# Optimization experiments

Measured on AMD Instinct MI355X. Metric: run time of the kernel, lower is better.

Reference implementation:

```python
import jax, jax.numpy as jnp
import numpy as np

N = 50000      # nodes
E = 800000     # edges (avg degree 16)
D = 96         # input_size == output_size
C = 10         # n_class
STEPS = 4      # num_layers -> GGNN propagation steps


def setup_inputs() -> dict:
    key = jax.random.key(0)
    ks = jax.random.split(key, 12)
    s = 1.0 / np.sqrt(D)
    return {
        "x": jax.random.normal(ks[0], (N, D), dtype=jnp.float32),
        "src": jax.random.randint(ks[1], (E,), 0, N, dtype=jnp.int32),
        "dst": jax.random.randint(ks[2], (E,), 0, N, dtype=jnp.int32),
        # edge message transform (DGL GatedGraphConv: Linear(out, out) per etype, 1 etype)
        "W_e": jax.random.normal(ks[3], (D, D), dtype=jnp.float32) * s,
        "b_e": jax.random.normal(ks[4], (D,), dtype=jnp.float32) * s,
        # GRUCell params (torch layout: rows ordered r, z, n)
        "W_ih": jax.random.normal(ks[5], (3 * D, D), dtype=jnp.float32) * s,
        "W_hh": jax.random.normal(ks[6], (3 * D, D), dtype=jnp.float32) * s,
        "b_ih": jax.random.normal(ks[7], (3 * D,), dtype=jnp.float32) * s,
        "b_hh": jax.random.normal(ks[8], (3 * D,), dtype=jnp.float32) * s,
        # classifier head
        "W_fc": jax.random.normal(ks[9], (C, D), dtype=jnp.float32) * s,
        "b_fc": jax.random.normal(ks[10], (C,), dtype=jnp.float32) * s,
    }


def _gru_cell(a, h, W_ih, W_hh, b_ih, b_hh):
    # torch.nn.GRUCell math; gate order r, z, n
    gx = a @ W_ih.T + b_ih            # [N, 3D]
    gh = h @ W_hh.T + b_hh            # [N, 3D]
    xr, xz, xn = jnp.split(gx, 3, axis=-1)
    hr, hz, hn = jnp.split(gh, 3, axis=-1)
    r = jax.nn.sigmoid(xr + hr)
    z = jax.nn.sigmoid(xz + hz)
    n = jnp.tanh(xn + r * hn)
    return (1.0 - z) * n + z * h


def reference(x, src, dst, W_e, b_e, W_ih, W_hh, b_ih, b_hh, W_fc, b_fc):
    h = x  # in_feats == out_feats, no padding needed
    for _ in range(STEPS):
        m = h @ W_e.T + b_e                                  # per-node transform [N, D]
        a = jax.ops.segment_sum(m[src], dst, num_segments=N) # gather + scatter-add [N, D]
        h = _gru_cell(a, h, W_ih, W_hh, b_ih, b_hh)
    logits = jax.nn.elu(h) @ W_fc.T + b_fc                   # [N, C]
    return logits
```

## Files before the change

kernel.cpp:

```cpp
#include <hip/hip_runtime.h>

static constexpr int D = 96;
static constexpr int G3 = 3 * D;
static constexpr int NSTEPS = 4;
static constexpr int NT = 18;
static constexpr int SCAN_BLK = 1024;
static constexpr int SLP = 104;
static constexpr int PLS = 97;
static constexpr int PLANE = 16 * PLS;

typedef __attribute__((ext_vector_type(8))) _Float16 f16x8;
typedef __attribute__((ext_vector_type(4))) _Float16 f16x4;
typedef __attribute__((ext_vector_type(4))) float f32x4;

__device__ __forceinline__ f16x8 load_a_frag(const _Float16* __restrict__ base,
                                             int r0, int lane, int kc) {
  int row = r0 + (lane & 15);
  int k0 = kc * 32 + ((lane >> 4) << 3);
  return *(const f16x8*)(base + (size_t)row * D + k0);
}

__device__ __forceinline__ f16x8 load_b_swz(const _Float16* __restrict__ W,
                                            int t, int kc, int lane) {
  return *(const f16x8*)(W + (((size_t)t * 3 + kc) * 64 + lane) * 8);
}


__global__ void convert_x_kernel(const float* __restrict__ x,
                                 _Float16* __restrict__ h, int total4) {
  int i = blockIdx.x * blockDim.x + threadIdx.x;
  if (i >= total4) return;
  float4 v = ((const float4*)x)[i];
  f16x4 o;
  o[0] = (_Float16)v.x; o[1] = (_Float16)v.y;
  o[2] = (_Float16)v.z; o[3] = (_Float16)v.w;
  *(f16x4*)(h + (size_t)i * 4) = o;
}

__global__ void compute_wx_kernel(const float* __restrict__ Wih,
                                  const float* __restrict__ We,
                                  const float* __restrict__ be,
                                  float* __restrict__ Wx,
                                  float* __restrict__ bxe) {
  int idx = blockIdx.x * blockDim.x + threadIdx.x;
  if (idx < G3 * D) {
    int r = idx / D, k = idx - r * D;
    float acc = 0.f;
    for (int c = 0; c < D; ++c) acc += Wih[r * D + c] * We[c * D + k];
    Wx[idx] = acc;
  } else if (idx < G3 * D + G3) {
    int r = idx - G3 * D;
    float acc = 0.f;
    for (int c = 0; c < D; ++c) acc += Wih[r * D + c] * be[c];
    bxe[r] = acc;
  }
}

__global__ void swizzle_f16_kernel(const float* __restrict__ Wx,
                                   const float* __restrict__ Whh,
                                   _Float16* __restrict__ WxF,
                                   _Float16* __restrict__ WhhF) {
  int idx = blockIdx.x * blockDim.x + threadIdx.x;
  if (idx >= 2 * NT * 3 * 64) return;
  int mat = idx / (NT * 3 * 64);
  int rem = idx - mat * (NT * 3 * 64);
  int t = rem / (3 * 64);
  int rem2 = rem - t * (3 * 64);
  int kc = rem2 >> 6;
  int lane = rem2 & 63;
  int c = t * 16 + (lane & 15);
  int k0 = kc * 32 + ((lane >> 4) << 3);
  const float* W = mat ? Whh : Wx;
  _Float16* dF = mat ? WhhF : WxF;
  f16x8 o;
#pragma unroll
  for (int j = 0; j < 8; ++j) o[j] = (_Float16)W[(size_t)c * D + k0 + j];
  *(f16x8*)(dF + (((size_t)t * 3 + kc) * 64 + lane) * 8) = o;
}


__global__ void hist_kernel(const int* __restrict__ dst, int* __restrict__ counts, int E) {
  int e = blockIdx.x * blockDim.x + threadIdx.x;
  if (e < E) atomicAdd(&counts[dst[e]], 1);
}

__global__ void partial_sum_kernel(const int* __restrict__ counts,
                                   int* __restrict__ blk_sums, int n) {
  __shared__ int red[256];
  int base = blockIdx.x * SCAN_BLK;
  int tid = threadIdx.x;
  int s = 0;
#pragma unroll
  for (int j = 0; j < 4; ++j) {
    int i = base + j * 256 + tid;
    if (i < n) s += counts[i];
  }
  red[tid] = s;
  __syncthreads();
  for (int off = 128; off > 0; off >>= 1) {
    if (tid < off) red[tid] += red[tid + off];
    __syncthreads();
  }
  if (tid == 0) blk_sums[blockIdx.x] = red[0];
}

__global__ void scan_offsets_kernel(const int* __restrict__ blk_sums,
                                    int* __restrict__ blk_off,
                                    int* __restrict__ row_ptr, int nb, int n) {
  __shared__ int lds[64];
  int tid = threadIdx.x;
  if (tid < nb) lds[tid] = blk_sums[tid];
  __syncthreads();
  if (tid == 0) {
    int run = 0;
    for (int i = 0; i < nb; ++i) { blk_off[i] = run; run += lds[i]; }
    row_ptr[n] = run;
  }
}

__global__ void block_scan_kernel(const int* __restrict__ counts,
                                  const int* __restrict__ blk_off,
                                  int* __restrict__ row_ptr, int n) {
  __shared__ int red[256];
  int base = blockIdx.x * SCAN_BLK;
  int tid = threadIdx.x;
  int i0 = base + tid * 4;
  int v0 = 0, v1 = 0, v2 = 0, v3 = 0;
  if (i0 + 3 < n) {
    int4 c = *(const int4*)(counts + i0);
    v0 = c.x; v1 = c.y; v2 = c.z; v3 = c.w;
  } else {
    if (i0 < n) v0 = counts[i0];
    if (i0 + 1 < n) v1 = counts[i0 + 1];
    if (i0 + 2 < n) v2 = counts[i0 + 2];
  }
  int tsum = v0 + v1 + v2 + v3;
  red[tid] = tsum;
  __syncthreads();
  for (int off = 1; off < 256; off <<= 1) {
    int t = (tid >= off) ? red[tid - off] : 0;
    __syncthreads();
    red[tid] += t;
    __syncthreads();
  }
  int excl = blk_off[blockIdx.x] + red[tid] - tsum;
  if (i0 < n) row_ptr[i0] = excl;
  if (i0 + 1 < n) row_ptr[i0 + 1] = excl + v0;
  if (i0 + 2 < n) row_ptr[i0 + 2] = excl + v0 + v1;
  if (i0 + 3 < n) row_ptr[i0 + 3] = excl + v0 + v1 + v2;
}

__global__ void fill_kernel(const int* __restrict__ src, const int* __restrict__ dst,
                            const int* __restrict__ row_ptr,
                            int* __restrict__ fillc,
                            unsigned short* __restrict__ csr_src, int E) {
  int e = blockIdx.x * blockDim.x + threadIdx.x;
  if (e >= E) return;
  int t = dst[e];
  int pos = row_ptr[t] + atomicAdd(&fillc[t], 1);
  csr_src[pos] = (unsigned short)src[e];
}


__device__ __forceinline__ void gru_epilogue(const float* lds,
                                             const _Float16* __restrict__ h,
                                             _Float16* __restrict__ hout,
                                             const int* __restrict__ row_ptr,
                                             const float* __restrict__ bxe,
                                             const float* __restrict__ bih,
                                             const float* __restrict__ bhh,
                                             int base_row, int tid) {
#pragma unroll
  for (int j = 0; j < 4; ++j) {
    int e = tid + j * 384;
    int row = e / D;
    int col = e - row * D;
    int grow = base_row + row;
    int a = row * PLS + col;
    float degf = (float)(row_ptr[grow + 1] - row_ptr[grow]);
    float R  = lds[a] + lds[PLANE + a];
    float Z  = lds[2 * PLANE + a] + lds[3 * PLANE + a];
    float XN = lds[4 * PLANE + a];
    float HN = lds[5 * PLANE + a];
    float rg = 1.0f / (1.0f + __expf(-(R + bih[col] + bhh[col] + degf * bxe[col])));
    float zg = 1.0f / (1.0f + __expf(-(Z + bih[D + col] + bhh[D + col] + degf * bxe[D + col])));
    float ng = tanhf(XN + bih[2 * D + col] + degf * bxe[2 * D + col] + rg * (HN + bhh[2 * D + col]));
    float hv = (float)h[(size_t)grow * D + col];
    hout[(size_t)grow * D + col] = (_Float16)((1.0f - zg) * ng + zg * hv);
  }
}

__global__ __launch_bounds__(384) void gru_fused_kernel(
    const _Float16* __restrict__ h, _Float16* __restrict__ hout,
    const int* __restrict__ row_ptr, const unsigned short* __restrict__ csr_src,
    const _Float16* __restrict__ WxF, const _Float16* __restrict__ WhhF,
    const float* __restrict__ bxe, const float* __restrict__ bih,
    const float* __restrict__ bhh, int n) {
  __shared__ float lds[6 * PLANE];
  _Float16* sl = (_Float16*)&lds[4 * PLANE];
  int r0 = blockIdx.x << 5;
  int tid = threadIdx.x;
  int w = tid >> 6;
  int lane = tid & 63;

  {
    int row = tid / 12;
    int part = tid - row * 12;
    int grow = r0 + row;
    float acc[8];
#pragma unroll
    for (int j = 0; j < 8; ++j) acc[j] = 0.f;
    if (grow < n) {
      int beg = row_ptr[grow], end = row_ptr[grow + 1];
      const _Float16* hp = h + (size_t)part * 8;
      int e = beg;
      for (; e + 7 < end; e += 8) {
        f16x8 v0 = *(const f16x8*)(hp + (size_t)csr_src[e] * D);
        f16x8 v1 = *(const f16x8*)(hp + (size_t)csr_src[e + 1] * D);
        f16x8 v2 = *(const f16x8*)(hp + (size_t)csr_src[e + 2] * D);
        f16x8 v3 = *(const f16x8*)(hp + (size_t)csr_src[e + 3] * D);
        f16x8 v4 = *(const f16x8*)(hp + (size_t)csr_src[e + 4] * D);
        f16x8 v5 = *(const f16x8*)(hp + (size_t)csr_src[e + 5] * D);
        f16x8 v6 = *(const f16x8*)(hp + (size_t)csr_src[e + 6] * D);
        f16x8 v7 = *(const f16x8*)(hp + (size_t)csr_src[e + 7] * D);
#pragma unroll
        for (int j = 0; j < 8; ++j)
          acc[j] += (((float)v0[j] + (float)v1[j]) + ((float)v2[j] + (float)v3[j])) +
                    (((float)v4[j] + (float)v5[j]) + ((float)v6[j] + (float)v7[j]));
      }
      if (e + 3 < end) {
        f16x8 v0 = *(const f16x8*)(hp + (size_t)csr_src[e] * D);
        f16x8 v1 = *(const f16x8*)(hp + (size_t)csr_src[e + 1] * D);
        f16x8 v2 = *(const f16x8*)(hp + (size_t)csr_src[e + 2] * D);
        f16x8 v3 = *(const f16x8*)(hp + (size_t)csr_src[e + 3] * D);
#pragma unroll
        for (int j = 0; j < 8; ++j)
          acc[j] += ((float)v0[j] + (float)v1[j]) + ((float)v2[j] + (float)v3[j]);
        e += 4;
      }
      for (; e < end; ++e) {
        f16x8 v = *(const f16x8*)(hp + (size_t)csr_src[e] * D);
#pragma unroll
        for (int j = 0; j < 8; ++j) acc[j] += (float)v[j];
      }
    }
    f16x8 o;
#pragma unroll
    for (int j = 0; j < 8; ++j) o[j] = (_Float16)acc[j];
    *(f16x8*)&sl[row * SLP + part * 8] = o;
  }
  __syncthreads();

  const int opS = (w < 3) ? 1 : 0;
  const _Float16* WF = opS ? WxF : WhhF;
  const int wg = opS ? w : (w - 3);
  const int t0 = wg * 6;
  const int plane = wg * 2 + (opS ? 0 : 1);

  f16x8 a0[3], a1[3];
  if (opS) {
#pragma unroll
    for (int kc = 0; kc < 3; ++kc) {
      int k0 = kc * 32 + ((lane >> 4) << 3);
      a0[kc] = *(const f16x8*)&sl[(lane & 15) * SLP + k0];
      a1[kc] = *(const f16x8*)&sl[(16 + (lane & 15)) * SLP + k0];
    }
  } else {
#pragma unroll
    for (int kc = 0; kc < 3; ++kc) {
      a0[kc] = load_a_frag(h, r0, lane, kc);
      a1[kc] = load_a_frag(h, r0 + 16, lane, kc);
    }
  }
  __syncthreads();

  f32x4 acc0[6], acc1[6];
#pragma unroll
  for (int t = 0; t < 6; ++t) {
    acc0[t] = (f32x4){0.f, 0.f, 0.f, 0.f};
    acc1[t] = (f32x4){0.f, 0.f, 0.f, 0.f};
  }

#pragma unroll
  for (int ct = 0; ct < 6; ++ct)
#pragma unroll
    for (int kc = 0; kc < 3; ++kc) {
      f16x8 b = load_b_swz(WF, t0 + ct, kc, lane);
      acc0[ct] = __builtin_amdgcn_mfma_f32_16x16x32_f16(a0[kc], b, acc0[ct], 0, 0, 0);
      acc1[ct] = __builtin_amdgcn_mfma_f32_16x16x32_f16(a1[kc], b, acc1[ct], 0, 0, 0);
    }

  int col_l = lane & 15;
  int rq = (lane >> 4) << 2;
#pragma unroll
  for (int ct = 0; ct < 6; ++ct)
#pragma unroll
    for (int q = 0; q < 4; ++q)
      lds[plane * PLANE + (rq + q) * PLS + ct * 16 + col_l] = acc0[ct][q];
  __syncthreads();
  gru_epilogue(lds, h, hout, row_ptr, bxe, bih, bhh, r0, tid);
  __syncthreads();
  if (r0 + 16 < n) {
#pragma unroll
    for (int ct = 0; ct < 6; ++ct)
#pragma unroll
      for (int q = 0; q < 4; ++q)
        lds[plane * PLANE + (rq + q) * PLS + ct * 16 + col_l] = acc1[ct][q];
    __syncthreads();
    gru_epilogue(lds, h, hout, row_ptr, bxe, bih, bhh, r0 + 16, tid);
  }
}

__global__ void head_kernel(const _Float16* __restrict__ h,
                            const float* __restrict__ Wfc,
                            const float* __restrict__ bfc,
                            float* __restrict__ out,
                            int n, int C) {
  int idx = blockIdx.x * blockDim.x + threadIdx.x;
  if (idx >= n * C) return;
  int i = idx / C;
  int c = idx - i * C;
  const _Float16* hr = h + (size_t)i * D;
  const float* wr = Wfc + (size_t)c * D;
  float acc = bfc[c];
#pragma unroll 8
  for (int k = 0; k < D; ++k) {
    float hv = (float)hr[k];
    float e = hv > 0.0f ? hv : (__expf(hv) - 1.0f);
    acc += e * wr[k];
  }
  out[idx] = acc;
}

extern "C" void kernel_launch(void* const* d_in, const int* in_sizes, int n_in,
                              void* d_out, int out_size, void* d_ws, size_t ws_size,
                              hipStream_t stream) {
  const float* x    = (const float*)d_in[0];
  const int*   src  = (const int*)d_in[1];
  const int*   dst  = (const int*)d_in[2];
  const float* W_e  = (const float*)d_in[3];
  const float* b_e  = (const float*)d_in[4];
  const float* W_ih = (const float*)d_in[5];
  const float* W_hh = (const float*)d_in[6];
  const float* b_ih = (const float*)d_in[7];
  const float* b_hh = (const float*)d_in[8];
  const float* W_fc = (const float*)d_in[9];
  const float* b_fc = (const float*)d_in[10];

  const int n = in_sizes[0] / D;
  const int E = in_sizes[1];
  const int C = out_size / n;

  _Float16* hA = (_Float16*)d_ws;
  _Float16* hB = hA + (size_t)n * D;
  float* Wx    = (float*)(hB + (size_t)n * D);
  _Float16* WxF  = (_Float16*)(Wx + (size_t)G3 * D);
  _Float16* WhhF = WxF + (size_t)G3 * D;
  float* bxe   = (float*)(WhhF + (size_t)G3 * D);
  int* counts  = (int*)(bxe + G3);
  int* fillc   = counts + n;
  int* row_ptr = fillc + n;
  unsigned short* csr_src = (unsigned short*)(row_ptr + (n + 1));
  int* blk_sums = (int*)(csr_src + E);
  int* blk_off  = blk_sums + 64;

  const int threads = 256;
  const int nb = (n + SCAN_BLK - 1) / SCAN_BLK;

  (void)hipMemsetAsync(counts, 0, (size_t)2 * n * sizeof(int), stream);
  hist_kernel<<<(E + threads - 1) / threads, threads, 0, stream>>>(dst, counts, E);
  partial_sum_kernel<<<nb, 256, 0, stream>>>(counts, blk_sums, n);
  scan_offsets_kernel<<<1, 64, 0, stream>>>(blk_sums, blk_off, row_ptr, nb, n);
  block_scan_kernel<<<nb, 256, 0, stream>>>(counts, blk_off, row_ptr, n);
  fill_kernel<<<(E + threads - 1) / threads, threads, 0, stream>>>(src, dst, row_ptr,
                                                                   fillc, csr_src, E);
  compute_wx_kernel<<<(G3 * D + G3 + threads - 1) / threads, threads, 0, stream>>>(
      W_ih, W_e, b_e, Wx, bxe);
  swizzle_f16_kernel<<<(2 * NT * 3 * 64 + threads - 1) / threads, threads, 0, stream>>>(
      Wx, W_hh, WxF, WhhF);
  convert_x_kernel<<<((n * D / 4) + threads - 1) / threads, threads, 0, stream>>>(
      x, hA, n * D / 4);

  const int gridG = (n + 31) / 32;

  const _Float16* hcur = hA;
  _Float16* hnext = hB;
  for (int step = 0; step < NSTEPS; ++step) {
    gru_fused_kernel<<<gridG, 384, 0, stream>>>(hcur, hnext, row_ptr, csr_src,
                                                WxF, WhhF, bxe, b_ih, b_hh, n);
    const _Float16* t = hcur; hcur = hnext; hnext = (_Float16*)t;
  }

  const int gridH = (n * C + threads - 1) / threads;
  head_kernel<<<gridH, threads, 0, stream>>>(hcur, W_fc, b_fc, (float*)d_out, n, C);
}
```

Baseline: 348.1 us.

## Compute GRU gates in registers per wave, dropping LDS staging of MFMA results

Reassigns the six waves so each owns a 16-column slice across all three gates, accumulating both the aggregated-input and hidden-state products into per-gate MFMA accumulators. The GRU epilogue now runs directly on accumulator registers instead of writing six float planes to LDS and reading them back after barriers. This shrinks LDS from about 37KB to about 6.6KB, which may allow more blocks per CU, and removes several __syncthreads. In exchange each wave loads more weight fragments and the hidden-state A fragments are reloaded per wave. Out-of-range rows are clamped on load and skipped on store.

```diff
diff --git a/kernel.cpp b/kernel.cpp
--- a/kernel.cpp
+++ b/kernel.cpp
@@ -6,16 +6,15 @@
 static constexpr int NT = 18;
 static constexpr int SCAN_BLK = 1024;
 static constexpr int SLP = 104;
-static constexpr int PLS = 97;
-static constexpr int PLANE = 16 * PLS;
 
 typedef __attribute__((ext_vector_type(8))) _Float16 f16x8;
 typedef __attribute__((ext_vector_type(4))) _Float16 f16x4;
 typedef __attribute__((ext_vector_type(4))) float f32x4;
 
-__device__ __forceinline__ f16x8 load_a_frag(const _Float16* __restrict__ base,
-                                             int r0, int lane, int kc) {
+__device__ __forceinline__ f16x8 load_a_frag_clamp(const _Float16* __restrict__ base,
+                                                   int r0, int lane, int kc, int n) {
   int row = r0 + (lane & 15);
+  if (row >= n) row = n - 1;
   int k0 = kc * 32 + ((lane >> 4) << 3);
   return *(const f16x8*)(base + (size_t)row * D + k0);
 }
@@ -162,42 +161,13 @@
 }
 
 
-__device__ __forceinline__ void gru_epilogue(const float* lds,
-                                             const _Float16* __restrict__ h,
-                                             _Float16* __restrict__ hout,
-                                             const int* __restrict__ row_ptr,
-                                             const float* __restrict__ bxe,
-                                             const float* __restrict__ bih,
-                                             const float* __restrict__ bhh,
-                                             int base_row, int tid) {
-#pragma unroll
-  for (int j = 0; j < 4; ++j) {
-    int e = tid + j * 384;
-    int row = e / D;
-    int col = e - row * D;
-    int grow = base_row + row;
-    int a = row * PLS + col;
-    float degf = (float)(row_ptr[grow + 1] - row_ptr[grow]);
-    float R  = lds[a] + lds[PLANE + a];
-    float Z  = lds[2 * PLANE + a] + lds[3 * PLANE + a];
-    float XN = lds[4 * PLANE + a];
-    float HN = lds[5 * PLANE + a];
-    float rg = 1.0f / (1.0f + __expf(-(R + bih[col] + bhh[col] + degf * bxe[col])));
-    float zg = 1.0f / (1.0f + __expf(-(Z + bih[D + col] + bhh[D + col] + degf * bxe[D + col])));
-    float ng = tanhf(XN + bih[2 * D + col] + degf * bxe[2 * D + col] + rg * (HN + bhh[2 * D + col]));
-    float hv = (float)h[(size_t)grow * D + col];
-    hout[(size_t)grow * D + col] = (_Float16)((1.0f - zg) * ng + zg * hv);
-  }
-}
-
 __global__ __launch_bounds__(384) void gru_fused_kernel(
     const _Float16* __restrict__ h, _Float16* __restrict__ hout,
     const int* __restrict__ row_ptr, const unsigned short* __restrict__ csr_src,
     const _Float16* __restrict__ WxF, const _Float16* __restrict__ WhhF,
     const float* __restrict__ bxe, const float* __restrict__ bih,
     const float* __restrict__ bhh, int n) {
-  __shared__ float lds[6 * PLANE];
-  _Float16* sl = (_Float16*)&lds[4 * PLANE];
+  __shared__ _Float16 sl[32 * SLP];
   int r0 = blockIdx.x << 5;
   int tid = threadIdx.x;
   int w = tid >> 6;
@@ -251,63 +221,52 @@
   }
   __syncthreads();
 
-  const int opS = (w < 3) ? 1 : 0;
-  const _Float16* WF = opS ? WxF : WhhF;
-  const int wg = opS ? w : (w - 3);
-  const int t0 = wg * 6;
-  const int plane = wg * 2 + (opS ? 0 : 1);
-
-  f16x8 a0[3], a1[3];
-  if (opS) {
+  const int t = w;
+  const int col_l = lane & 15;
+  const int rq = (lane >> 4) << 2;
+  const int col = t * 16 + col_l;
+
+  const float br  = bih[col] + bhh[col];
+  const float bz  = bih[D + col] + bhh[D + col];
+  const float bxn = bih[2 * D + col];
+  const float bhn = bhh[2 * D + col];
+  const float xr = bxe[col], xz = bxe[D + col], xnc = bxe[2 * D + col];
+
+#pragma unroll
+  for (int rt = 0; rt < 2; ++rt) {
+    const int rbase = r0 + rt * 16;
+    f16x8 aS[3], aH[3];
 #pragma unroll
     for (int kc = 0; kc < 3; ++kc) {
       int k0 = kc * 32 + ((lane >> 4) << 3);
-      a0[kc] = *(const f16x8*)&sl[(lane & 15) * SLP + k0];
-      a1[kc] = *(const f16x8*)&sl[(16 + (lane & 15)) * SLP + k0];
+      aS[kc] = *(const f16x8*)&sl[(rt * 16 + (lane & 15)) * SLP + k0];
+      aH[kc] = load_a_frag_clamp(h, rbase, lane, kc, n);
     }
-  } else {
+    f32x4 accR = {0.f, 0.f, 0.f, 0.f};
+    f32x4 accZ = {0.f, 0.f, 0.f, 0.f};
+    f32x4 accXN = {0.f, 0.f, 0.f, 0.f};
+    f32x4 accHN = {0.f, 0.f, 0.f, 0.f};
 #pragma unroll
     for (int kc = 0; kc < 3; ++kc) {
-      a0[kc] = load_a_frag(h, r0, lane, kc);
-      a1[kc] = load_a_frag(h, r0 + 16, lane, kc);
+      accR  = __builtin_amdgcn_mfma_f32_16x16x32_f16(aS[kc], load_b_swz(WxF,  t,      kc, lane), accR, 0, 0, 0);
+      accR  = __builtin_amdgcn_mfma_f32_16x16x32_f16(aH[kc], load_b_swz(WhhF, t,      kc, lane), accR, 0, 0, 0);
+      accZ  = __builtin_amdgcn_mfma_f32_16x16x32_f16(aS[kc], load_b_swz(WxF,  6 + t,  kc, lane), accZ, 0, 0, 0);
+      accZ  = __builtin_amdgcn_mfma_f32_16x16x32_f16(aH[kc], load_b_swz(WhhF, 6 + t,  kc, lane), accZ, 0, 0, 0);
+      accXN = __builtin_amdgcn_mfma_f32_16x16x32_f16(aS[kc], load_b_swz(WxF,  12 + t, kc, lane), accXN, 0, 0, 0);
+      accHN = __builtin_amdgcn_mfma_f32_16x16x32_f16(aH[kc], load_b_swz(WhhF, 12 + t, kc, lane), accHN, 0, 0, 0);
     }
-  }
-  __syncthreads();
-
-  f32x4 acc0[6], acc1[6];
-#pragma unroll
-  for (int t = 0; t < 6; ++t) {
-    acc0[t] = (f32x4){0.f, 0.f, 0.f, 0.f};
-    acc1[t] = (f32x4){0.f, 0.f, 0.f, 0.f};
-  }
-
-#pragma unroll
-  for (int ct = 0; ct < 6; ++ct)
-#pragma unroll
-    for (int kc = 0; kc < 3; ++kc) {
-      f16x8 b = load_b_swz(WF, t0 + ct, kc, lane);
-      acc0[ct] = __builtin_amdgcn_mfma_f32_16x16x32_f16(a0[kc], b, acc0[ct], 0, 0, 0);
-      acc1[ct] = __builtin_amdgcn_mfma_f32_16x16x32_f16(a1[kc], b, acc1[ct], 0, 0, 0);
+#pragma unroll
+    for (int q = 0; q < 4; ++q) {
+      int grow = rbase + rq + q;
+      if (grow < n) {
+        float degf = (float)(row_ptr[grow + 1] - row_ptr[grow]);
+        float rg = 1.0f / (1.0f + __expf(-(accR[q] + br + degf * xr)));
+        float zg = 1.0f / (1.0f + __expf(-(accZ[q] + bz + degf * xz)));
+        float ng = tanhf(accXN[q] + bxn + degf * xnc + rg * (accHN[q] + bhn));
+        float hv = (float)h[(size_t)grow * D + col];
+        hout[(size_t)grow * D + col] = (_Float16)((1.0f - zg) * ng + zg * hv);
+      }
     }
-
-  int col_l = lane & 15;
-  int rq = (lane >> 4) << 2;
-#pragma unroll
-  for (int ct = 0; ct < 6; ++ct)
-#pragma unroll
-    for (int q = 0; q < 4; ++q)
-      lds[plane * PLANE + (rq + q) * PLS + ct * 16 + col_l] = acc0[ct][q];
-  __syncthreads();
-  gru_epilogue(lds, h, hout, row_ptr, bxe, bih, bhh, r0, tid);
-  __syncthreads();
-  if (r0 + 16 < n) {
-#pragma unroll
-    for (int ct = 0; ct < 6; ++ct)
-#pragma unroll
-      for (int q = 0; q < 4; ++q)
-        lds[plane * PLANE + (rq + q) * PLS + ct * 16 + col_l] = acc1[ct][q];
-    __syncthreads();
-    gru_epilogue(lds, h, hout, row_ptr, bxe, bih, bhh, r0 + 16, tid);
   }
 }
 
```

New measurement: 353.2 us. No clear change (+1.5%).

## Replace global-atomic CSR fill with two-pass bucketed routing and local fill

Applied to the files above, without the earlier changes.

The per-edge global atomic fill of the CSR source array is replaced by two passes. First, edges are routed into 1024-node buckets in a staging buffer, using shared-memory counters and one global atomic per bucket per block. Second, each bucket is scattered into its final CSR slot using shared-memory atomics. This removes contention and scattered global atomics at the cost of an extra kernel launch and a pass over a staging buffer.

```diff
diff --git a/kernel.cpp b/kernel.cpp
--- a/kernel.cpp
+++ b/kernel.cpp
@@ -150,15 +150,68 @@
   if (i0 + 3 < n) row_ptr[i0 + 3] = excl + v0 + v1 + v2;
 }
 
-__global__ void fill_kernel(const int* __restrict__ src, const int* __restrict__ dst,
-                            const int* __restrict__ row_ptr,
-                            int* __restrict__ fillc,
-                            unsigned short* __restrict__ csr_src, int E) {
-  int e = blockIdx.x * blockDim.x + threadIdx.x;
-  if (e >= E) return;
-  int t = dst[e];
-  int pos = row_ptr[t] + atomicAdd(&fillc[t], 1);
-  csr_src[pos] = (unsigned short)src[e];
+__global__ void route_kernel(const int* __restrict__ src, const int* __restrict__ dst,
+                             const int* __restrict__ row_ptr,
+                             int* __restrict__ bucket_fill,
+                             unsigned* __restrict__ stage, int E, int n) {
+  __shared__ int cnt[64], gbase[64], rpb[64];
+  int tid = threadIdx.x;
+  int base = blockIdx.x * 1024;
+  if (tid < 64) {
+    cnt[tid] = 0;
+    int node = tid << 10;
+    rpb[tid] = row_ptr[node < n ? node : n];
+  }
+  __syncthreads();
+  int b[4], lp[4], sv[4], dl[4];
+#pragma unroll
+  for (int j = 0; j < 4; ++j) {
+    int e = base + tid * 4 + j;
+    if (e < E) {
+      sv[j] = src[e];
+      int d = dst[e];
+      b[j] = d >> 10;
+      dl[j] = d & 1023;
+      lp[j] = atomicAdd(&cnt[b[j]], 1);
+    } else {
+      b[j] = -1;
+    }
+  }
+  __syncthreads();
+  if (tid < 64) {
+    int c = cnt[tid];
+    gbase[tid] = (c > 0) ? atomicAdd(&bucket_fill[tid], c) : 0;
+  }
+  __syncthreads();
+#pragma unroll
+  for (int j = 0; j < 4; ++j) {
+    if (b[j] >= 0) {
+      int pos = rpb[b[j]] + gbase[b[j]] + lp[j];
+      stage[pos] = (unsigned)sv[j] | ((unsigned)dl[j] << 16);
+    }
+  }
+}
+
+__global__ void local_fill_kernel(const unsigned* __restrict__ stage,
+                                  const int* __restrict__ row_ptr,
+                                  unsigned short* __restrict__ csr_src, int n) {
+  __shared__ int rp[1024];
+  __shared__ int lf[1024];
+  int b = blockIdx.x;
+  int node0 = b << 10;
+  int nn = n - node0; if (nn > 1024) nn = 1024;
+  int tid = threadIdx.x;
+  if (tid < nn) { rp[tid] = row_ptr[node0 + tid]; lf[tid] = 0; }
+  __syncthreads();
+  int ebeg = row_ptr[node0];
+  int eend = row_ptr[node0 + nn];
+  for (int i = ebeg + tid; i < eend; i += 1024) {
+    unsigned p = stage[i];
+    int dl = p >> 16;
+    int s = p & 0xFFFF;
+    int pos = rp[dl] + atomicAdd(&lf[dl], 1);
+    csr_src[pos] = (unsigned short)s;
+  }
 }
 
 
@@ -358,22 +411,25 @@
   _Float16* WhhF = WxF + (size_t)G3 * D;
   float* bxe   = (float*)(WhhF + (size_t)G3 * D);
   int* counts  = (int*)(bxe + G3);
-  int* fillc   = counts + n;
-  int* row_ptr = fillc + n;
+  int* bucket_fill = counts + n;
+  int* row_ptr = bucket_fill + n;
   unsigned short* csr_src = (unsigned short*)(row_ptr + (n + 1));
   int* blk_sums = (int*)(csr_src + E);
   int* blk_off  = blk_sums + 64;
+  unsigned* stage = (unsigned*)(blk_off + 64);
 
   const int threads = 256;
   const int nb = (n + SCAN_BLK - 1) / SCAN_BLK;
+  const int NB = (n + 1023) >> 10;
 
   (void)hipMemsetAsync(counts, 0, (size_t)2 * n * sizeof(int), stream);
   hist_kernel<<<(E + threads - 1) / threads, threads, 0, stream>>>(dst, counts, E);
   partial_sum_kernel<<<nb, 256, 0, stream>>>(counts, blk_sums, n);
   scan_offsets_kernel<<<1, 64, 0, stream>>>(blk_sums, blk_off, row_ptr, nb, n);
   block_scan_kernel<<<nb, 256, 0, stream>>>(counts, blk_off, row_ptr, n);
-  fill_kernel<<<(E + threads - 1) / threads, threads, 0, stream>>>(src, dst, row_ptr,
-                                                                   fillc, csr_src, E);
+  route_kernel<<<(E + 1023) / 1024, 256, 0, stream>>>(src, dst, row_ptr,
+                                                      bucket_fill, stage, E, n);
+  local_fill_kernel<<<NB, 1024, 0, stream>>>(stage, row_ptr, csr_src, n);
   compute_wx_kernel<<<(G3 * D + G3 + threads - 1) / threads, threads, 0, stream>>>(
       W_ih, W_e, b_e, Wx, bxe);
   swizzle_f16_kernel<<<(2 * NT * 3 * 64 + threads - 1) / threads, threads, 0, stream>>>(
```

New measurement: 342.2 us. About the same (-1.7%).
